# Kernel tuning notes

Measured on AMD Instinct MI355X. Metric: run time of the kernel, lower is better.

Reference implementation:

```python
import jax, jax.numpy as jnp
import numpy as np

B, T, H = 128, 1024, 512


def setup_inputs() -> dict:
    key = jax.random.key(0)
    ks = jax.random.split(key, 4)
    vel = jax.random.normal(ks[0], (B, T, 2), dtype=jnp.float32)
    # weight_ih ~ N(0, sqrt(1/2)); weight_hh orthogonal; biases zero; output zeroed
    # (we use random output weights so fwd output is non-trivial for testing)
    W_ih = jax.random.normal(ks[1], (H, 2), dtype=jnp.float32) * np.sqrt(0.5)
    A = jax.random.normal(ks[2], (H, H), dtype=jnp.float32)
    Q, _ = jnp.linalg.qr(A)
    W_hh = Q.astype(jnp.float32)
    b_ih = jnp.zeros((H,), dtype=jnp.float32)
    b_hh = jnp.zeros((H,), dtype=jnp.float32)
    W_out = jax.random.normal(ks[3], (2, H), dtype=jnp.float32) * 0.05
    b_out = jnp.zeros((2,), dtype=jnp.float32)
    return {"vel": vel, "W_ih": W_ih, "W_hh": W_hh, "b_ih": b_ih,
            "b_hh": b_hh, "W_out": W_out, "b_out": b_out}


def reference(vel, W_ih, W_hh, b_ih, b_hh, W_out, b_out):
    # Precompute input projection for all timesteps: [B, T, H]
    x_proj = jnp.einsum('btc,hc->bth', vel, W_ih) + b_ih + b_hh
    x_tbh = jnp.swapaxes(x_proj, 0, 1)  # [T, B, H] for scan over time

    def step(h, x_t):
        # h: [B, H]; x_t: [B, H]
        h_new = jnp.tanh(x_t + h @ W_hh.T)
        return h_new, h_new

    h0 = jnp.zeros((vel.shape[0], W_hh.shape[0]), dtype=vel.dtype)
    _, u_tbh = jax.lax.scan(step, h0, x_tbh)
    u_vals = jnp.swapaxes(u_tbh, 0, 1)  # [B, T, H]
    pos_est = jnp.einsum('bth,oh->bto', u_vals, W_out) + b_out  # [B, T, 2]
    return pos_est, u_vals
```

## Files before the change

kernel.cpp:

```cpp
#include <hip/hip_runtime.h>
#include <hip/hip_bf16.h>


#define TT 1024
#define BB 128
#define HH 512

typedef short s16x8 __attribute__((ext_vector_type(8)));
typedef float f32x4 __attribute__((ext_vector_type(4)));
typedef unsigned int uint;
typedef unsigned short ushort_t;
typedef unsigned long long u64;

#define MFMA_B16(a, b, c) __builtin_amdgcn_mfma_f32_16x16x32_bf16((a), (b), (c), 0, 0, 0)

__device__ __forceinline__ ushort_t bf16_rne(float f) {
  uint u = __float_as_uint(f);
  u += 0x7fffu + ((u >> 16) & 1u);
  return (ushort_t)(u >> 16);
}

__device__ __forceinline__ float tanh_fast(float z) {
  float e = __expf(2.0f * z);
  return 1.0f - 2.0f * __builtin_amdgcn_rcpf(e + 1.0f);
}

__global__ __launch_bounds__(256) void rnn_kernel(
    const float* __restrict__ vel, const float* __restrict__ W_ih,
    const float* __restrict__ W_hh, const float* __restrict__ b_ih,
    const float* __restrict__ b_hh, float* __restrict__ u_out,
    uint* __restrict__ flags, u64* __restrict__ pub) {
  __shared__ uint4 hlds_mem[2048];
  char* hlds = (char*)hlds_mem;

  const int tid = threadIdx.x;
  const int lane = tid & 63;
  const int w = tid >> 6;
  const int c = blockIdx.x & 7;
  const int i = blockIdx.x >> 3;
  const int l15 = lane & 15;
  const int kg = lane >> 4;
  const int n_g = i * 64 + w * 16 + l15;

  s16x8 wreg[16];
#pragma unroll
  for (int kt = 0; kt < 16; ++kt) {
    const float* wp = W_hh + (size_t)n_g * HH + kt * 32 + kg * 8;
    float4 lo = *(const float4*)wp;
    float4 hi = *(const float4*)(wp + 4);
    s16x8 s;
    s[0] = (short)bf16_rne(lo.x); s[1] = (short)bf16_rne(lo.y);
    s[2] = (short)bf16_rne(lo.z); s[3] = (short)bf16_rne(lo.w);
    s[4] = (short)bf16_rne(hi.x); s[5] = (short)bf16_rne(hi.y);
    s[6] = (short)bf16_rne(hi.z); s[7] = (short)bf16_rne(hi.w);
    wreg[kt] = s;
  }
  const float wih0 = W_ih[n_g * 2 + 0];
  const float wih1 = W_ih[n_g * 2 + 1];
  const float bsum = b_ih[n_g] + b_hh[n_g];

  {
    uint4 z = {0u, 0u, 0u, 0u};
    uint4* p = (uint4*)(hlds + tid * 64);
    p[0] = z; p[1] = z; p[2] = z; p[3] = z;
  }
  __syncthreads();

  const f32x4 z4 = {0.f, 0.f, 0.f, 0.f};
  for (int t = 0; t < TT; ++t) {
    const int cur = t & 1;
    const int nxt = cur ^ 1;

    float2 v[4];
#pragma unroll
    for (int r = 0; r < 4; ++r)
      v[r] = *(const float2*)(vel + ((size_t)(c * 16 + kg * 4 + r) * TT + t) * 2);

    f32x4 a0 = z4, a1 = z4, a2 = z4, a3 = z4;
#pragma unroll
    for (int kt = 0; kt < 16; kt += 4) {
      uint base = (uint)cur * 16384u + (uint)l15 * 1024u + (uint)kg * 16u;
      uint swz = ((uint)l15 & 7u) << 4;
      s16x8 f0 = *(const s16x8*)(hlds + ((base + (uint)(kt + 0) * 64u) ^ swz));
      s16x8 f1 = *(const s16x8*)(hlds + ((base + (uint)(kt + 1) * 64u) ^ swz));
      s16x8 f2 = *(const s16x8*)(hlds + ((base + (uint)(kt + 2) * 64u) ^ swz));
      s16x8 f3 = *(const s16x8*)(hlds + ((base + (uint)(kt + 3) * 64u) ^ swz));
      a0 = MFMA_B16(f0, wreg[kt + 0], a0);
      a1 = MFMA_B16(f1, wreg[kt + 1], a1);
      a2 = MFMA_B16(f2, wreg[kt + 2], a2);
      a3 = MFMA_B16(f3, wreg[kt + 3], a3);
    }
    f32x4 acc = (a0 + a1) + (a2 + a3);

    float uv[4];
    u64 pk = 0;
#pragma unroll
    for (int r = 0; r < 4; ++r) {
      float x = fmaf(v[r].x, wih0, fmaf(v[r].y, wih1, bsum));
      float uval = tanh_fast(x + acc[r]);
      uv[r] = uval;
      pk |= (u64)bf16_rne(uval) << (16 * r);
    }

    if (t == TT - 1) {
#pragma unroll
      for (int r = 0; r < 4; ++r)
        __builtin_nontemporal_store(
            uv[r], u_out + ((size_t)(c * 16 + kg * 4 + r) * TT + t) * HH + n_g);
      break;
    }

    const int par = nxt;

    {
      u64* dst = pub + (((size_t)par * 8 + c) * 8 + i) * 256 + (w * 16 + l15) * 4 + kg;
      __hip_atomic_store(dst, pk, __ATOMIC_RELAXED, __HIP_MEMORY_SCOPE_AGENT);
    }
    asm volatile("s_waitcnt vmcnt(0)" ::: "memory");
    if (lane == 0)
      __hip_atomic_store(&flags[(c * 8 + i) * 4 + w], (uint)(t + 1),
                         __ATOMIC_RELAXED, __HIP_MEMORY_SCOPE_AGENT);

#pragma unroll
    for (int r = 0; r < 4; ++r) {
      int b = kg * 4 + r;
      __builtin_nontemporal_store(
          uv[r], u_out + ((size_t)(c * 16 + b) * TT + t) * HH + n_g);
      uint logical = (uint)nxt * 16384u + (uint)b * 1024u + (uint)n_g * 2u;
      *(ushort_t*)(hlds + (logical ^ (((uint)b & 7u) << 4))) =
          (ushort_t)(pk >> (16 * r));
    }

    {
      int jj = lane >> 2;
      int j = jj + (jj >= i ? 1 : 0);
      int fw = lane & 3;
      const uint tgt = (uint)(t + 1);
      while (true) {
        uint f = (lane < 28)
                     ? __hip_atomic_load(&flags[(c * 8 + j) * 4 + fw],
                                         __ATOMIC_RELAXED, __HIP_MEMORY_SCOPE_AGENT)
                     : 0xFFFFFFFFu;
        if (__all((int)(f >= tgt))) break;
      }
      asm volatile("" ::: "memory");
    }

    {
      const int col = tid >> 2;
      const int rq = tid & 3;
      u64 g[7];
#pragma unroll
      for (int s7 = 0; s7 < 7; ++s7) {
        int j = s7 + (s7 >= i ? 1 : 0);
        g[s7] = __hip_atomic_load(
            pub + (((size_t)par * 8 + c) * 8 + j) * 256 + col * 4 + rq,
            __ATOMIC_RELAXED, __HIP_MEMORY_SCOPE_AGENT);
      }
#pragma unroll
      for (int s7 = 0; s7 < 7; ++s7) {
        int j = s7 + (s7 >= i ? 1 : 0);
        uint n = (uint)(j * 64 + col);
#pragma unroll
        for (int e = 0; e < 4; ++e) {
          uint b = (uint)(rq * 4 + e);
          uint logical = (uint)nxt * 16384u + b * 1024u + n * 2u;
          *(ushort_t*)(hlds + (logical ^ ((b & 7u) << 4))) =
              (ushort_t)(g[s7] >> (16 * e));
        }
      }
    }
    __syncthreads();
  }
}

__global__ void init_kernel(uint* flags) {
  __hip_atomic_store(&flags[threadIdx.x], 0u, __ATOMIC_RELAXED,
                     __HIP_MEMORY_SCOPE_AGENT);
}

__global__ __launch_bounds__(256) void pos_kernel(const float* __restrict__ u,
                                                  const float* __restrict__ W_out,
                                                  const float* __restrict__ b_out,
                                                  float* __restrict__ pos) {
  int row = blockIdx.x * 4 + (threadIdx.x >> 6);
  int lane = threadIdx.x & 63;
  const float* ur = u + (size_t)row * HH + lane * 8;
  float4 u0 = *(const float4*)ur;
  float4 u1 = *(const float4*)(ur + 4);
  float4 w00 = *(const float4*)(W_out + lane * 8);
  float4 w01 = *(const float4*)(W_out + lane * 8 + 4);
  float4 w10 = *(const float4*)(W_out + HH + lane * 8);
  float4 w11 = *(const float4*)(W_out + HH + lane * 8 + 4);
  float p0 = u0.x * w00.x + u0.y * w00.y + u0.z * w00.z + u0.w * w00.w +
             u1.x * w01.x + u1.y * w01.y + u1.z * w01.z + u1.w * w01.w;
  float p1 = u0.x * w10.x + u0.y * w10.y + u0.z * w10.z + u0.w * w10.w +
             u1.x * w11.x + u1.y * w11.y + u1.z * w11.z + u1.w * w11.w;
#pragma unroll
  for (int off = 32; off; off >>= 1) {
    p0 += __shfl_xor(p0, off);
    p1 += __shfl_xor(p1, off);
  }
  if (lane == 0) {
    pos[(size_t)row * 2 + 0] = p0 + b_out[0];
    pos[(size_t)row * 2 + 1] = p1 + b_out[1];
  }
}

extern "C" void kernel_launch(void* const* d_in, const int* in_sizes, int n_in,
                              void* d_out, int out_size, void* d_ws, size_t ws_size,
                              hipStream_t stream) {
  const float* vel   = (const float*)d_in[0];
  const float* W_ih  = (const float*)d_in[1];
  const float* W_hh  = (const float*)d_in[2];
  const float* b_ih  = (const float*)d_in[3];
  const float* b_hh  = (const float*)d_in[4];
  const float* W_out = (const float*)d_in[5];
  const float* b_out = (const float*)d_in[6];

  float* pos = (float*)d_out;
  float* u   = pos + (size_t)BB * TT * 2;

  uint* flags = (uint*)d_ws;
  u64* pub = (u64*)((char*)d_ws + 4096);

  init_kernel<<<1, 256, 0, stream>>>(flags);
  rnn_kernel<<<64, 256, 0, stream>>>(vel, W_ih, W_hh, b_ih, b_hh, u, flags, pub);
  pos_kernel<<<(BB * TT) / 4, 256, 0, stream>>>(u, W_out, b_out, pos);
}
```

Measured before the change: 2.255 ms.

## Split hidden dim over 4 blocks per batch group with tagged-data sync and local-first MFMA

Cuts the grid from 64 to 32 blocks, so each block now computes 128 hidden units across 2 MFMA N-tiles and only 4 peer blocks exchange state per batch group. The separate flag array is dropped: each published value carries the timestep in its upper 32 bits, so readers spin directly on the data instead of on flags. The MFMAs over the block's own hidden slice run before waiting on remote data, which overlaps local compute with the exchange. This lowers global synchronisation traffic and latency, at the cost of fewer CUs in use and twice the MFMA work per block.

```diff
diff --git a/kernel.cpp b/kernel.cpp
--- a/kernel.cpp
+++ b/kernel.cpp
@@ -13,23 +13,36 @@
 typedef unsigned long long u64;
 
 #define MFMA_B16(a, b, c) __builtin_amdgcn_mfma_f32_16x16x32_bf16((a), (b), (c), 0, 0, 0)
-
-__device__ __forceinline__ ushort_t bf16_rne(float f) {
+#define ALD(p) __hip_atomic_load((p), __ATOMIC_RELAXED, __HIP_MEMORY_SCOPE_AGENT)
+#define AST(p, v) __hip_atomic_store((p), (v), __ATOMIC_RELAXED, __HIP_MEMORY_SCOPE_AGENT)
+
+static __device__ __forceinline__ ushort_t bf16_rne(float f) {
   uint u = __float_as_uint(f);
   u += 0x7fffu + ((u >> 16) & 1u);
   return (ushort_t)(u >> 16);
 }
 
-__device__ __forceinline__ float tanh_fast(float z) {
+static __device__ __forceinline__ float tanh_fast(float z) {
   float e = __expf(2.0f * z);
   return 1.0f - 2.0f * __builtin_amdgcn_rcpf(e + 1.0f);
+}
+
+static __device__ __forceinline__ s16x8 packW(const float* wp) {
+  float4 lo = *(const float4*)wp;
+  float4 hi = *(const float4*)(wp + 4);
+  s16x8 s;
+  s[0] = (short)bf16_rne(lo.x); s[1] = (short)bf16_rne(lo.y);
+  s[2] = (short)bf16_rne(lo.z); s[3] = (short)bf16_rne(lo.w);
+  s[4] = (short)bf16_rne(hi.x); s[5] = (short)bf16_rne(hi.y);
+  s[6] = (short)bf16_rne(hi.z); s[7] = (short)bf16_rne(hi.w);
+  return s;
 }
 
 __global__ __launch_bounds__(256) void rnn_kernel(
     const float* __restrict__ vel, const float* __restrict__ W_ih,
     const float* __restrict__ W_hh, const float* __restrict__ b_ih,
     const float* __restrict__ b_hh, float* __restrict__ u_out,
-    uint* __restrict__ flags, u64* __restrict__ pub) {
+    u64* __restrict__ pub) {
   __shared__ uint4 hlds_mem[2048];
   char* hlds = (char*)hlds_mem;
 
@@ -37,146 +50,172 @@
   const int lane = tid & 63;
   const int w = tid >> 6;
   const int c = blockIdx.x & 7;
-  const int i = blockIdx.x >> 3;
+  const int p = blockIdx.x >> 3;
   const int l15 = lane & 15;
   const int kg = lane >> 4;
-  const int n_g = i * 64 + w * 16 + l15;
-
-  s16x8 wreg[16];
-#pragma unroll
-  for (int kt = 0; kt < 16; ++kt) {
-    const float* wp = W_hh + (size_t)n_g * HH + kt * 32 + kg * 8;
-    float4 lo = *(const float4*)wp;
-    float4 hi = *(const float4*)(wp + 4);
-    s16x8 s;
-    s[0] = (short)bf16_rne(lo.x); s[1] = (short)bf16_rne(lo.y);
-    s[2] = (short)bf16_rne(lo.z); s[3] = (short)bf16_rne(lo.w);
-    s[4] = (short)bf16_rne(hi.x); s[5] = (short)bf16_rne(hi.y);
-    s[6] = (short)bf16_rne(hi.z); s[7] = (short)bf16_rne(hi.w);
-    wreg[kt] = s;
-  }
-  const float wih0 = W_ih[n_g * 2 + 0];
-  const float wih1 = W_ih[n_g * 2 + 1];
-  const float bsum = b_ih[n_g] + b_hh[n_g];
+  const int n0 = p * 128 + w * 32;
+  const uint swz = ((uint)l15 & 7u) << 4;
+
+  s16x8 wl[2][4], wr[2][12];
+#pragma unroll
+  for (int nt = 0; nt < 2; ++nt) {
+    const float* wb = W_hh + (size_t)(n0 + nt * 16 + l15) * HH + kg * 8;
+#pragma unroll
+    for (int kk = 0; kk < 4; ++kk)
+      wl[nt][kk] = packW(wb + (p * 4 + kk) * 32);
+#pragma unroll
+    for (int j = 0; j < 12; ++j)
+      wr[nt][j] = packW(wb + (((p * 4 + 4 + j) & 15)) * 32);
+  }
+  float wih0[2], wih1[2], bs[2];
+#pragma unroll
+  for (int nt = 0; nt < 2; ++nt) {
+    int n = n0 + nt * 16 + l15;
+    wih0[nt] = W_ih[n * 2 + 0];
+    wih1[nt] = W_ih[n * 2 + 1];
+    bs[nt] = b_ih[n] + b_hh[n];
+  }
 
   {
     uint4 z = {0u, 0u, 0u, 0u};
-    uint4* p = (uint4*)(hlds + tid * 64);
-    p[0] = z; p[1] = z; p[2] = z; p[3] = z;
+    uint4* zp = (uint4*)(hlds + tid * 64);
+    zp[0] = z; zp[1] = z; zp[2] = z; zp[3] = z;
   }
   __syncthreads();
 
   const f32x4 z4 = {0.f, 0.f, 0.f, 0.f};
+  const int ps0 = (p + 1) & 3, ps1 = (p + 2) & 3, ps2 = (p + 3) & 3;
+  const uint remoff = (uint)(p * 256 + 256);
+
   for (int t = 0; t < TT; ++t) {
     const int cur = t & 1;
     const int nxt = cur ^ 1;
 
+    u64 g00 = 0, g01 = 0, g02 = 0, g03 = 0;
+    u64 g10 = 0, g11 = 0, g12 = 0, g13 = 0;
+    u64 g20 = 0, g21 = 0, g22 = 0, g23 = 0;
+    const u64* sp0 = pub + ((size_t)(cur * 8 + c) * 4 + ps0) * 1024 + tid * 4;
+    const u64* sp1 = pub + ((size_t)(cur * 8 + c) * 4 + ps1) * 1024 + tid * 4;
+    const u64* sp2 = pub + ((size_t)(cur * 8 + c) * 4 + ps2) * 1024 + tid * 4;
+    if (t > 0) {
+      g00 = ALD(sp0); g01 = ALD(sp0 + 1); g02 = ALD(sp0 + 2); g03 = ALD(sp0 + 3);
+      g10 = ALD(sp1); g11 = ALD(sp1 + 1); g12 = ALD(sp1 + 2); g13 = ALD(sp1 + 3);
+      g20 = ALD(sp2); g21 = ALD(sp2 + 1); g22 = ALD(sp2 + 2); g23 = ALD(sp2 + 3);
+      asm volatile("" ::: "memory");
+    }
+
     float2 v[4];
 #pragma unroll
     for (int r = 0; r < 4; ++r)
       v[r] = *(const float2*)(vel + ((size_t)(c * 16 + kg * 4 + r) * TT + t) * 2);
 
-    f32x4 a0 = z4, a1 = z4, a2 = z4, a3 = z4;
-#pragma unroll
-    for (int kt = 0; kt < 16; kt += 4) {
-      uint base = (uint)cur * 16384u + (uint)l15 * 1024u + (uint)kg * 16u;
-      uint swz = ((uint)l15 & 7u) << 4;
-      s16x8 f0 = *(const s16x8*)(hlds + ((base + (uint)(kt + 0) * 64u) ^ swz));
-      s16x8 f1 = *(const s16x8*)(hlds + ((base + (uint)(kt + 1) * 64u) ^ swz));
-      s16x8 f2 = *(const s16x8*)(hlds + ((base + (uint)(kt + 2) * 64u) ^ swz));
-      s16x8 f3 = *(const s16x8*)(hlds + ((base + (uint)(kt + 3) * 64u) ^ swz));
-      a0 = MFMA_B16(f0, wreg[kt + 0], a0);
-      a1 = MFMA_B16(f1, wreg[kt + 1], a1);
-      a2 = MFMA_B16(f2, wreg[kt + 2], a2);
-      a3 = MFMA_B16(f3, wreg[kt + 3], a3);
-    }
-    f32x4 acc = (a0 + a1) + (a2 + a3);
-
-    float uv[4];
-    u64 pk = 0;
+    f32x4 a00 = z4, a01 = z4, a10 = z4, a11 = z4;
+    const uint abase = (uint)cur * 16384u + (uint)l15 * 1024u + (uint)kg * 16u;
+#pragma unroll
+    for (int kk = 0; kk < 4; ++kk) {
+      s16x8 f = *(const s16x8*)(hlds + ((abase + (uint)(p * 256 + kk * 64)) ^ swz));
+      if (kk & 1) { a01 = MFMA_B16(f, wl[0][kk], a01); a11 = MFMA_B16(f, wl[1][kk], a11); }
+      else        { a00 = MFMA_B16(f, wl[0][kk], a00); a10 = MFMA_B16(f, wl[1][kk], a10); }
+    }
+
+    if (t > 0) {
+      const uint tgt = (uint)t;
+      const uint grow = (uint)tid >> 4;
+      const uint gb = ((uint)cur * 16384u + grow * 1024u + (((uint)tid << 2) & 63u) * 4u) ^
+                      ((grow & 7u) << 4);
+      while (true) {
+        uint mn = min(min((uint)(g00 >> 32), (uint)(g01 >> 32)),
+                      min((uint)(g02 >> 32), (uint)(g03 >> 32)));
+        if (mn >= tgt) break;
+        g00 = ALD(sp0); g01 = ALD(sp0 + 1); g02 = ALD(sp0 + 2); g03 = ALD(sp0 + 3);
+      }
+      { uint4 d = {(uint)g00, (uint)g01, (uint)g02, (uint)g03};
+        *(uint4*)(hlds + (gb ^ ((uint)ps0 * 256u))) = d; }
+      while (true) {
+        uint mn = min(min((uint)(g10 >> 32), (uint)(g11 >> 32)),
+                      min((uint)(g12 >> 32), (uint)(g13 >> 32)));
+        if (mn >= tgt) break;
+        g10 = ALD(sp1); g11 = ALD(sp1 + 1); g12 = ALD(sp1 + 2); g13 = ALD(sp1 + 3);
+      }
+      { uint4 d = {(uint)g10, (uint)g11, (uint)g12, (uint)g13};
+        *(uint4*)(hlds + (gb ^ ((uint)ps1 * 256u))) = d; }
+      while (true) {
+        uint mn = min(min((uint)(g20 >> 32), (uint)(g21 >> 32)),
+                      min((uint)(g22 >> 32), (uint)(g23 >> 32)));
+        if (mn >= tgt) break;
+        g20 = ALD(sp2); g21 = ALD(sp2 + 1); g22 = ALD(sp2 + 2); g23 = ALD(sp2 + 3);
+      }
+      { uint4 d = {(uint)g20, (uint)g21, (uint)g22, (uint)g23};
+        *(uint4*)(hlds + (gb ^ ((uint)ps2 * 256u))) = d; }
+      __syncthreads();
+    }
+
+#pragma unroll
+    for (int j = 0; j < 12; ++j) {
+      uint off = (remoff + (uint)(j * 64)) & 1023u;
+      s16x8 f = *(const s16x8*)(hlds + ((abase + off) ^ swz));
+      if (j & 1) { a01 = MFMA_B16(f, wr[0][j], a01); a11 = MFMA_B16(f, wr[1][j], a11); }
+      else       { a00 = MFMA_B16(f, wr[0][j], a00); a10 = MFMA_B16(f, wr[1][j], a10); }
+    }
+    f32x4 acc0 = a00 + a01;
+    f32x4 acc1 = a10 + a11;
+
+    float uv0[4], uv1[4];
+    ushort_t hb0[4], hb1[4];
 #pragma unroll
     for (int r = 0; r < 4; ++r) {
-      float x = fmaf(v[r].x, wih0, fmaf(v[r].y, wih1, bsum));
-      float uval = tanh_fast(x + acc[r]);
-      uv[r] = uval;
-      pk |= (u64)bf16_rne(uval) << (16 * r);
-    }
-
-    if (t == TT - 1) {
-#pragma unroll
-      for (int r = 0; r < 4; ++r)
-        __builtin_nontemporal_store(
-            uv[r], u_out + ((size_t)(c * 16 + kg * 4 + r) * TT + t) * HH + n_g);
-      break;
-    }
-
-    const int par = nxt;
-
-    {
-      u64* dst = pub + (((size_t)par * 8 + c) * 8 + i) * 256 + (w * 16 + l15) * 4 + kg;
-      __hip_atomic_store(dst, pk, __ATOMIC_RELAXED, __HIP_MEMORY_SCOPE_AGENT);
-    }
-    asm volatile("s_waitcnt vmcnt(0)" ::: "memory");
-    if (lane == 0)
-      __hip_atomic_store(&flags[(c * 8 + i) * 4 + w], (uint)(t + 1),
-                         __ATOMIC_RELAXED, __HIP_MEMORY_SCOPE_AGENT);
+      float x0 = fmaf(v[r].x, wih0[0], fmaf(v[r].y, wih1[0], bs[0]));
+      float x1 = fmaf(v[r].x, wih0[1], fmaf(v[r].y, wih1[1], bs[1]));
+      uv0[r] = tanh_fast(x0 + acc0[r]);
+      uv1[r] = tanh_fast(x1 + acc1[r]);
+      hb0[r] = bf16_rne(uv0[r]);
+      hb1[r] = bf16_rne(uv1[r]);
+    }
+
+    if (t < TT - 1) {
+      const bool odd = (l15 & 1) != 0;
+      const uint rowbase = (uint)(kg * 4) + (odd ? 2u : 0u);
+      const uint cpq = (uint)(w * 16) + ((uint)l15 >> 1);
+      u64* dpb = pub + ((size_t)(nxt * 8 + c) * 4 + p) * 1024;
+      const u64 tagw = (u64)(uint)(t + 1) << 32;
+      const uint ldsb = (uint)nxt * 16384u;
+#pragma unroll
+      for (int nt = 0; nt < 2; ++nt) {
+        const ushort_t* hb = nt ? hb1 : hb0;
+        uint a01p = (uint)hb[0] | ((uint)hb[1] << 16);
+        uint a23p = (uint)hb[2] | ((uint)hb[3] << 16);
+        uint b01p = __shfl_xor(a01p, 1);
+        uint b23p = __shfl_xor(a23p, 1);
+        uint eP = odd ? b23p : a01p;
+        uint oP = odd ? a23p : b01p;
+        uint pr0 = (eP & 0xFFFFu) | (oP << 16);
+        uint pr1 = (eP >> 16) | (oP & 0xFFFF0000u);
+        uint cp = cpq + (uint)(nt * 8);
+        AST(dpb + rowbase * 64 + cp, (u64)pr0 | tagw);
+        AST(dpb + (rowbase + 1) * 64 + cp, (u64)pr1 | tagw);
+        uint cb = (uint)(n0 + nt * 16 + (l15 & ~1)) * 2u;
+        *(uint*)(hlds + ((ldsb + rowbase * 1024u + cb) ^ ((rowbase & 7u) << 4))) = pr0;
+        *(uint*)(hlds + ((ldsb + (rowbase + 1) * 1024u + cb) ^ (((rowbase + 1) & 7u) << 4))) = pr1;
+      }
+    }
 
 #pragma unroll
     for (int r = 0; r < 4; ++r) {
-      int b = kg * 4 + r;
-      __builtin_nontemporal_store(
-          uv[r], u_out + ((size_t)(c * 16 + b) * TT + t) * HH + n_g);
-      uint logical = (uint)nxt * 16384u + (uint)b * 1024u + (uint)n_g * 2u;
-      *(ushort_t*)(hlds + (logical ^ (((uint)b & 7u) << 4))) =
-          (ushort_t)(pk >> (16 * r));
-    }
-
-    {
-      int jj = lane >> 2;
-      int j = jj + (jj >= i ? 1 : 0);
-      int fw = lane & 3;
-      const uint tgt = (uint)(t + 1);
-      while (true) {
-        uint f = (lane < 28)
-                     ? __hip_atomic_load(&flags[(c * 8 + j) * 4 + fw],
-                                         __ATOMIC_RELAXED, __HIP_MEMORY_SCOPE_AGENT)
-                     : 0xFFFFFFFFu;
-        if (__all((int)(f >= tgt))) break;
-      }
-      asm volatile("" ::: "memory");
-    }
-
-    {
-      const int col = tid >> 2;
-      const int rq = tid & 3;
-      u64 g[7];
-#pragma unroll
-      for (int s7 = 0; s7 < 7; ++s7) {
-        int j = s7 + (s7 >= i ? 1 : 0);
-        g[s7] = __hip_atomic_load(
-            pub + (((size_t)par * 8 + c) * 8 + j) * 256 + col * 4 + rq,
-            __ATOMIC_RELAXED, __HIP_MEMORY_SCOPE_AGENT);
-      }
-#pragma unroll
-      for (int s7 = 0; s7 < 7; ++s7) {
-        int j = s7 + (s7 >= i ? 1 : 0);
-        uint n = (uint)(j * 64 + col);
-#pragma unroll
-        for (int e = 0; e < 4; ++e) {
-          uint b = (uint)(rq * 4 + e);
-          uint logical = (uint)nxt * 16384u + b * 1024u + n * 2u;
-          *(ushort_t*)(hlds + (logical ^ ((b & 7u) << 4))) =
-              (ushort_t)(g[s7] >> (16 * e));
-        }
-      }
-    }
+      size_t ub = ((size_t)(c * 16 + kg * 4 + r) * TT + t) * HH;
+      __builtin_nontemporal_store(uv0[r], u_out + ub + n0 + l15);
+      __builtin_nontemporal_store(uv1[r], u_out + ub + n0 + 16 + l15);
+    }
+
+    if (t == TT - 1) break;
     __syncthreads();
   }
 }
 
-__global__ void init_kernel(uint* flags) {
-  __hip_atomic_store(&flags[threadIdx.x], 0u, __ATOMIC_RELAXED,
-                     __HIP_MEMORY_SCOPE_AGENT);
+__global__ void init_kernel(u64* pub) {
+  int idx = (blockIdx.x * 256 + threadIdx.x) * 4;
+#pragma unroll
+  for (int k = 0; k < 4; ++k)
+    __hip_atomic_store(&pub[idx + k], 0ull, __ATOMIC_RELAXED, __HIP_MEMORY_SCOPE_AGENT);
 }
 
 __global__ __launch_bounds__(256) void pos_kernel(const float* __restrict__ u,
@@ -221,10 +260,9 @@
   float* pos = (float*)d_out;
   float* u   = pos + (size_t)BB * TT * 2;
 
-  uint* flags = (uint*)d_ws;
-  u64* pub = (u64*)((char*)d_ws + 4096);
-
-  init_kernel<<<1, 256, 0, stream>>>(flags);
-  rnn_kernel<<<64, 256, 0, stream>>>(vel, W_ih, W_hh, b_ih, b_hh, u, flags, pub);
+  u64* pub = (u64*)d_ws;
+
+  init_kernel<<<64, 256, 0, stream>>>(pub);
+  rnn_kernel<<<32, 256, 0, stream>>>(vel, W_ih, W_hh, b_ih, b_hh, u, pub);
   pos_kernel<<<(BB * TT) / 4, 256, 0, stream>>>(u, W_out, b_out, pos);
 }
```

After: 2.245 ms. About the same (-0.4%).
